# Performance work log

Measured on AMD Instinct MI355X. Metric: run time of the kernel, lower is better.

The kernel has to match this reference:

```python
import jax, jax.numpy as jnp
import numpy as np

V, D, S, L, H, R, W = 32000, 512, 1536, 4, 4, 32, 128
HFF = int(2.0 * D)
N = S + 1          # anchor node at index 0 + S tokens
K = W + 2          # anchor edge + (W+1) causal window edges
LN_EPS = 1e-5


def _layer_norm(x, g, b):
    m = jnp.mean(x, axis=-1, keepdims=True)
    v = jnp.mean((x - m) ** 2, axis=-1, keepdims=True)
    return (x - m) * jax.lax.rsqrt(v + LN_EPS) * g + b


def _neighbors():
    # windowed causal neighborhood: node i sees nodes i-W..i, plus anchor (node 0)
    pos = jnp.arange(N)
    offs = jnp.arange(-W, 1)                     # W+1 offsets
    idx_w = pos[:, None] + offs[None, :]         # [N, W+1]
    valid_w = idx_w >= 0
    idx_w = jnp.maximum(idx_w, 0)
    anchor_valid = (pos > W)[:, None]            # avoid double-counting anchor when already in window
    idx = jnp.concatenate([jnp.zeros((N, 1), idx_w.dtype), idx_w], axis=1)   # [N, K]
    mask = jnp.concatenate([anchor_valid, valid_w], axis=1)                  # [N, K]
    return idx, mask


def setup_inputs() -> dict:
    key = jax.random.key(0)
    ks = jax.random.split(key, 10)
    std = 0.02
    return {
        'input_ids': jax.random.randint(ks[0], (1, S), 0, V),
        'embed': jax.random.normal(ks[1], (V, D), jnp.float32) * std,
        'pos_emb': jax.random.normal(ks[2], (S, D), jnp.float32) * std,
        'ln_in_g': jnp.ones((D,), jnp.float32),
        'ln_in_b': jnp.zeros((D,), jnp.float32),
        'anchor_state': jnp.zeros((), jnp.float32),
        'anchor_val': jax.random.normal(ks[3], (D,), jnp.float32) * std,
        'state_w': jax.random.normal(ks[4], (D,), jnp.float32) * std,
        'state_b': jnp.zeros((), jnp.float32),
        'wq': jax.random.normal(ks[5], (L, H, D, R), jnp.float32) * std,
        'wk': jax.random.normal(ks[6], (L, H, D, R), jnp.float32) * std,
        'gate': jnp.full((L,), 0.1, jnp.float32),
        'ln_g': jnp.ones((L, D), jnp.float32),
        'ln_b': jnp.zeros((L, D), jnp.float32),
        'ffn_w1': jax.random.normal(ks[7], (L, D, HFF), jnp.float32) * std,
        'ffn_b1': jnp.zeros((L, HFF), jnp.float32),
        'ffn_w2': jax.random.normal(ks[8], (L, HFF, D), jnp.float32) * std,
        'ffn_b2': jnp.zeros((L, D), jnp.float32),
        'ln2_g': jnp.ones((L, D), jnp.float32),
        'ln2_b': jnp.zeros((L, D), jnp.float32),
    }


def reference(input_ids, embed, pos_emb, ln_in_g, ln_in_b, anchor_state, anchor_val,
              state_w, state_b, wq, wk, gate, ln_g, ln_b,
              ffn_w1, ffn_b1, ffn_w2, ffn_b2, ln2_g, ln2_b):
    B = input_ids.shape[0]
    # token embedding + learned position encoding + input norm
    tok = embed[input_ids] + pos_emb[None]                 # [B,S,D]
    tok = _layer_norm(tok, ln_in_g, ln_in_b)
    tok_state = tok @ state_w + state_b                    # [B,S] scalar state per node
    # prepend anchor node
    val = jnp.concatenate([jnp.broadcast_to(anchor_val, (B, 1, D)), tok], axis=1)       # [B,N,D]
    state = jnp.concatenate([jnp.broadcast_to(anchor_state, (B, 1)), tok_state], axis=1)  # [B,N]
    idx, mask = _neighbors()
    scale = 1.0 / np.sqrt(R)
    for l in range(L):
        # low-rank multi-head pairwise scores on windowed neighborhood
        q = jnp.einsum('bnd,hdr->bnhr', val, wq[l])
        k = jnp.einsum('bnd,hdr->bnhr', val, wk[l])
        kg = k[:, idx]                                     # [B,N,K,H,R] gather
        s = jnp.einsum('bnhr,bnkhr->bnkh', q, kg) * scale  # [B,N,K,H]
        # signed_smoothmax head aggregation
        hw = jax.nn.softmax(jnp.abs(s), axis=-1)
        a = jnp.sum(s * hw, axis=-1)                       # [B,N,K]
        # signed_abs_softmax edge compression over neighborhood
        absa = jnp.where(mask[None], jnp.abs(a), -jnp.inf)
        e = jnp.sign(a) * jax.nn.softmax(absa, axis=-1)    # masked entries -> 0 weight
        # state-weighted edges
        sg = state[:, idx]                                 # [B,N,K]
        e = e * sg
        val_g = val[:, idx]                                # [B,N,K,D]
        d_val = jnp.einsum('bnk,bnkd->bnd', e, val_g)
        d_state = jnp.sum(e, axis=-1)
        # gated residual + post-norm
        state = state + gate[l] * d_state
        val = val + gate[l] * d_val
        val = _layer_norm(val, ln_g[l], ln_b[l])
        # value feed-forward (pre-norm, residual scale 1.0)
        h = jax.nn.gelu(_layer_norm(val, ln2_g[l], ln2_b[l]) @ ffn_w1[l] + ffn_b1[l], approximate=False)
        val = val + h @ ffn_w2[l] + ffn_b2[l]
    return val
```

## Files before the change

kernel.cpp:

```cpp
#include <hip/hip_runtime.h>
#include <hip/hip_bf16.h>

namespace {

constexpr int D    = 512;
constexpr int S    = 1536;
constexpr int N    = S + 1;
constexpr int L    = 4;
constexpr int H    = 4;
constexpr int R    = 32;
constexpr int W    = 128;
constexpr int HFF  = 1024;
constexpr float EPS = 1e-5f;

constexpr int TB   = 4;
constexpr int NB4  = (N + TB - 1) / TB;
constexpr int SP   = 133;
constexpr int SPAD = 136;

typedef __attribute__((ext_vector_type(8))) short short8;
typedef __attribute__((ext_vector_type(4))) float floatx4;

__device__ inline ushort f2bf(float x){
  __hip_bfloat16 h = __float2bfloat16(x);
  return *reinterpret_cast<ushort*>(&h);
}
__device__ inline float bf2f(uint u){
  union { uint u; float f; } c; c.u = u << 16; return c.f;
}

__device__ inline float wave_sum(float v){
#pragma unroll
  for (int o = 32; o; o >>= 1) v += __shfl_xor(v, o, 64);
  return v;
}
__device__ inline float wave_max(float v){
#pragma unroll
  for (int o = 32; o; o >>= 1) v = fmaxf(v, __shfl_xor(v, o, 64));
  return v;
}
__device__ inline float block_sum(float v, float* scr){
  v = wave_sum(v);
  __syncthreads();
  if ((threadIdx.x & 63) == 0) scr[threadIdx.x >> 6] = v;
  __syncthreads();
  return scr[0] + scr[1] + scr[2] + scr[3];
}

__global__ __launch_bounds__(256) void pack_wqk_bf(const float* __restrict__ wq,
                                                   const float* __restrict__ wk,
                                                   ushort* __restrict__ out){
  int i = blockIdx.x * 256 + threadIdx.x;
  int d = i & 511;
  int c = (i >> 9) & 255;
  int l = i >> 17;
  int cc = c & 127;
  int h = cc >> 5, r = cc & 31;
  const float* src = (c < 128) ? wq : wk;
  out[i] = f2bf(src[((l * H + h) * D + d) * R + r]);
}

__global__ __launch_bounds__(256) void transpose_bf(const float* __restrict__ src,
                                                    ushort* __restrict__ dst,
                                                    int rows, int cols){
  __shared__ float tile[32][33];
  const float* s = src + (size_t)blockIdx.z * rows * cols;
  ushort* d = dst + (size_t)blockIdx.z * rows * cols;
  int c0 = blockIdx.x * 32, r0 = blockIdx.y * 32;
  int tx = threadIdx.x & 31, ty = threadIdx.x >> 5;
  for (int rr = ty; rr < 32; rr += 8)
    tile[rr][tx] = s[(size_t)(r0 + rr) * cols + c0 + tx];
  __syncthreads();
  for (int rr = ty; rr < 32; rr += 8)
    d[(size_t)(c0 + rr) * rows + r0 + tx] = f2bf(tile[tx][rr]);
}

__global__ __launch_bounds__(256) void embed_ln_kernel(
    const int* __restrict__ ids, const float* __restrict__ embed,
    const float* __restrict__ pos, const float* __restrict__ g,
    const float* __restrict__ b, const float* __restrict__ anchor_val,
    const float* __restrict__ anchor_state, const float* __restrict__ state_w,
    const float* __restrict__ state_b, float* __restrict__ val,
    ushort* __restrict__ valbf, float* __restrict__ state)
{
  __shared__ float scr[4];
  int n = blockIdx.x, t = threadIdx.x;
  if (n == 0){
    float a0 = anchor_val[t], a1 = anchor_val[t + 256];
    val[t] = a0; val[t + 256] = a1;
    valbf[t] = f2bf(a0); valbf[t + 256] = f2bf(a1);
    if (t == 0) state[0] = anchor_state[0];
    return;
  }
  int tp = n - 1;
  int id = ids[tp];
  float x0 = embed[(size_t)id * D + t]       + pos[tp * D + t];
  float x1 = embed[(size_t)id * D + t + 256] + pos[tp * D + t + 256];
  float mean = block_sum(x0 + x1, scr) * (1.f / D);
  float var  = block_sum(x0 * x0 + x1 * x1, scr) * (1.f / D) - mean * mean;
  float rs   = rsqrtf(var + EPS);
  float y0 = (x0 - mean) * rs * g[t]       + b[t];
  float y1 = (x1 - mean) * rs * g[t + 256] + b[t + 256];
  val[n * D + t]       = y0;
  val[n * D + t + 256] = y1;
  valbf[n * D + t]       = f2bf(y0);
  valbf[n * D + t + 256] = f2bf(y1);
  float ts = block_sum(y0 * state_w[t] + y1 * state_w[t + 256], scr);
  if (t == 0) state[n] = ts + state_b[0];
}

template<int ACT>
__global__ __launch_bounds__(256) void gemm_bf16(
    const ushort* __restrict__ A, const ushort* __restrict__ Bt,
    const float* __restrict__ bias, const float* __restrict__ resid,
    float* __restrict__ C, ushort* __restrict__ Cbf,
    int M, int Kd, int Nc)
{
  constexpr int SLAB = 272;
  __shared__ ushort As[8 * SLAB];
  __shared__ ushort Bs[8 * SLAB];
  int row0 = blockIdx.y * 32;
  int col0 = blockIdx.x * 32;
  int t = threadIdx.x;
  int lane = t & 63, w = t >> 6;
  int wr = w & 1, wc = w >> 1;
  int q = lane >> 4, lm = lane & 15;

  int srow = t >> 3, skb = t & 7;
  int arow = min(row0 + srow, M - 1);
  const ushort* ag = A  + (size_t)arow * Kd + skb * 8;
  const ushort* bg = Bt + (size_t)(col0 + srow) * Kd + skb * 8;
  ushort* as = &As[skb * SLAB + srow * 8];
  ushort* bs = &Bs[skb * SLAB + srow * 8];

  const ushort* ar = &As[(wr * 16 + lm) * 8];
  const ushort* br = &Bs[(wc * 16 + lm) * 8];

  floatx4 acc = {0.f, 0.f, 0.f, 0.f};

  for (int k0 = 0; k0 < Kd; k0 += 64){
    uint4 av = *(const uint4*)(ag + k0);
    uint4 bv = *(const uint4*)(bg + k0);
    *(uint4*)as = av;
    *(uint4*)bs = bv;
    __syncthreads();
#pragma unroll
    for (int kk = 0; kk < 2; ++kk){
      short8 a = *(const short8*)(ar + (kk * 4 + q) * SLAB);
      short8 b = *(const short8*)(br + (kk * 4 + q) * SLAB);
      acc = __builtin_amdgcn_mfma_f32_16x16x32_bf16(a, b, acc, 0, 0, 0);
    }
    __syncthreads();
  }

  int col = col0 + wc * 16 + lm;
#pragma unroll
  for (int r = 0; r < 4; ++r){
    int row = row0 + wr * 16 + q * 4 + r;
    if (row >= M) continue;
    float v = acc[r] + (bias ? bias[col] : 0.f);
    if (ACT == 1) v = 0.5f * v * (1.f + erff(v * 0.70710678118654752f));
    if (resid) v += resid[(size_t)row * Nc + col];
    size_t o = (size_t)row * Nc + col;
    if (C)   C[o] = v;
    if (Cbf) Cbf[o] = f2bf(v);
  }
}

__global__ __launch_bounds__(256) void attn4_kernel(
    const ushort* __restrict__ qkbf, const float* __restrict__ val0,
    const ushort* __restrict__ val0bf, const float* __restrict__ state_in,
    float* __restrict__ val1, ushort* __restrict__ x2bf,
    float* __restrict__ state_out,
    const float* __restrict__ gate_p, const float* __restrict__ lng,
    const float* __restrict__ lnb, const float* __restrict__ ln2g,
    const float* __restrict__ ln2b)
{
  __shared__ float kg[64 * SPAD];
  __shared__ float qsh[TB * 128];
  __shared__ float ssh[16 * SPAD];
  __shared__ float ash[TB * SPAD];
  const int n0 = blockIdx.x * TB;
  const int t = threadIdx.x;
  const int w = t >> 6, l = t & 63;
  const float gate = gate_p[0];
  const float scale = 0.17677669529663687f;

#pragma unroll
  for (int i = t; i < TB * 128; i += 256){
    int it = i >> 7, ch = i & 127;
    int gr = min(n0 + it, N - 1);
    qsh[i] = bf2f((uint)qkbf[(size_t)gr * 256 + ch]);
  }

  for (int half = 0; half < 2; ++half){
    for (int i = t; i < SP * 16; i += 256){
      int c = i >> 4, c4 = i & 15;
      int g = (c == 132) ? 0 : min(max(n0 - W + c, 0), N - 1);
      uint2 v = *(const uint2*)&qkbf[(size_t)g * 256 + 128 + half * 64 + c4 * 4];
      int ch = c4 * 4;
      kg[(ch + 0) * SPAD + c] = bf2f(v.x & 0xffffu);
      kg[(ch + 1) * SPAD + c] = bf2f(v.x >> 16);
      kg[(ch + 2) * SPAD + c] = bf2f(v.y & 0xffffu);
      kg[(ch + 3) * SPAD + c] = bf2f(v.y >> 16);
    }
    __syncthreads();
    for (int tk = t; tk < TB * 2 * SP; tk += 256){
      int c = tk % SP;
      int th = tk / SP;
      int tok = th & 3, hh = th >> 2;
      int h = half * 2 + hh;
      const float* qs = &qsh[tok * 128 + h * 32];
      const float* ks = &kg[hh * 32 * SPAD + c];
      float acc = 0.f;
#pragma unroll
      for (int r = 0; r < 32; ++r) acc += qs[r] * ks[r * SPAD];
      ssh[(tok * 4 + h) * SPAD + c] = acc * scale;
    }
    __syncthreads();
  }

  for (int i = t; i < TB * SP; i += 256){
    int tok = i / SP, c = i - tok * SP;
    const float* sr = &ssh[tok * 4 * SPAD + c];
    float s0 = sr[0], s1 = sr[SPAD], s2 = sr[2 * SPAD], s3 = sr[3 * SPAD];
    float a0 = fabsf(s0), a1 = fabsf(s1), a2 = fabsf(s2), a3 = fabsf(s3);
    float m = fmaxf(fmaxf(a0, a1), fmaxf(a2, a3));
    float w0 = expf(a0 - m), w1 = expf(a1 - m), w2 = expf(a2 - m), w3 = expf(a3 - m);
    ash[tok * SPAD + c] = (s0 * w0 + s1 * w1 + s2 * w2 + s3 * w3) / (w0 + w1 + w2 + w3);
  }
  __syncthreads();

  {
    const int n = n0 + w;
    float* arow = &ash[w * SPAD];
    float a0 = arow[l];
    float a1 = arow[64 + l];
    float a2 = (l < 5) ? arow[128 + l] : 0.f;
    bool ok0 = (l >= w) && (n0 - W + l >= 0);
    bool ok1 = (n0 - W + 64 + l >= 0);
    bool ok2;
    if (l < 4)       ok2 = (l <= w);
    else if (l == 4) ok2 = (n > W);
    else             ok2 = false;
    float cand = -3.4e38f;
    if (ok0) cand = fabsf(a0);
    if (ok1) cand = fmaxf(cand, fabsf(a1));
    if (ok2) cand = fmaxf(cand, fabsf(a2));
    float m = wave_max(cand);
    float e0 = ok0 ? expf(fabsf(a0) - m) : 0.f;
    float e1 = ok1 ? expf(fabsf(a1) - m) : 0.f;
    float e2 = ok2 ? expf(fabsf(a2) - m) : 0.f;
    float inv = 1.f / wave_sum(e0 + e1 + e2);
    int g0 = min(max(n0 - W + l, 0), N - 1);
    int g1 = min(max(n0 - W + 64 + l, 0), N - 1);
    int g2 = (l < 4) ? min(n0 + l, N - 1) : 0;
    float sg0 = (a0 > 0.f) ? 1.f : ((a0 < 0.f) ? -1.f : 0.f);
    float sg1 = (a1 > 0.f) ? 1.f : ((a1 < 0.f) ? -1.f : 0.f);
    float sg2 = (a2 > 0.f) ? 1.f : ((a2 < 0.f) ? -1.f : 0.f);
    float t0 = sg0 * e0 * inv * state_in[g0];
    float t1 = sg1 * e1 * inv * state_in[g1];
    float t2 = (l < 5) ? sg2 * e2 * inv * state_in[g2] : 0.f;
    arow[l] = t0;
    arow[64 + l] = t1;
    if (l < 5) arow[128 + l] = t2;
    float ds = wave_sum(t0 + t1 + t2);
    if (l == 0 && n < N) state_out[n] = state_in[n] + gate * ds;
  }
  __syncthreads();

  float acc[TB][2];
#pragma unroll
  for (int k = 0; k < TB; ++k){ acc[k][0] = 0.f; acc[k][1] = 0.f; }
  {
    const int d0 = 2 * t;
    for (int c = 0; c < SP; ++c){
      int g = (c == 132) ? 0 : min(max(n0 - W + c, 0), N - 1);
      uint v = *(const uint*)&val0bf[(size_t)g * D + d0];
      float vx = bf2f(v & 0xffffu), vy = bf2f(v >> 16);
#pragma unroll
      for (int k = 0; k < TB; ++k){
        float e = ash[k * SPAD + c];
        acc[k][0] += e * vx;
        acc[k][1] += e * vy;
      }
    }
  }
  float* xbuf = kg;
  {
    const int d0 = 2 * t;
#pragma unroll
    for (int k = 0; k < TB; ++k){
      int nc = min(n0 + k, N - 1);
      float2 vv = *(const float2*)&val0[(size_t)nc * D + d0];
      xbuf[k * 520 + d0]     = vv.x + gate * acc[k][0];
      xbuf[k * 520 + d0 + 1] = vv.y + gate * acc[k][1];
    }
  }
  __syncthreads();

  {
    const int n = n0 + w;
    const int d = l * 8;
    const float* xr = &xbuf[w * 520 + d];
    float x[8];
#pragma unroll
    for (int j = 0; j < 8; ++j) x[j] = xr[j];
    float s1 = 0.f, s2 = 0.f;
#pragma unroll
    for (int j = 0; j < 8; ++j){ s1 += x[j]; s2 += x[j] * x[j]; }
    s1 = wave_sum(s1); s2 = wave_sum(s2);
    float mean = s1 * (1.f / D);
    float var  = s2 * (1.f / D) - mean * mean;
    float rs   = rsqrtf(var + EPS);
    float y[8];
    float u1 = 0.f, u2 = 0.f;
#pragma unroll
    for (int j = 0; j < 8; ++j){
      float yv = (x[j] - mean) * rs * lng[d + j] + lnb[d + j];
      y[j] = yv; u1 += yv; u2 += yv * yv;
    }
    u1 = wave_sum(u1); u2 = wave_sum(u2);
    float mean2 = u1 * (1.f / D);
    float var2  = u2 * (1.f / D) - mean2 * mean2;
    float rs2   = rsqrtf(var2 + EPS);
    if (n < N){
      *(float4*)&val1[(size_t)n * D + d]     = make_float4(y[0], y[1], y[2], y[3]);
      *(float4*)&val1[(size_t)n * D + d + 4] = make_float4(y[4], y[5], y[6], y[7]);
      uint4 pk;
      uint z0 = f2bf((y[0] - mean2) * rs2 * ln2g[d + 0] + ln2b[d + 0]);
      uint z1 = f2bf((y[1] - mean2) * rs2 * ln2g[d + 1] + ln2b[d + 1]);
      uint z2 = f2bf((y[2] - mean2) * rs2 * ln2g[d + 2] + ln2b[d + 2]);
      uint z3 = f2bf((y[3] - mean2) * rs2 * ln2g[d + 3] + ln2b[d + 3]);
      uint z4 = f2bf((y[4] - mean2) * rs2 * ln2g[d + 4] + ln2b[d + 4]);
      uint z5 = f2bf((y[5] - mean2) * rs2 * ln2g[d + 5] + ln2b[d + 5]);
      uint z6 = f2bf((y[6] - mean2) * rs2 * ln2g[d + 6] + ln2b[d + 6]);
      uint z7 = f2bf((y[7] - mean2) * rs2 * ln2g[d + 7] + ln2b[d + 7]);
      pk.x = z0 | (z1 << 16); pk.y = z2 | (z3 << 16);
      pk.z = z4 | (z5 << 16); pk.w = z6 | (z7 << 16);
      *(uint4*)&x2bf[(size_t)n * D + d] = pk;
    }
  }
}

}

extern "C" void kernel_launch(void* const* d_in, const int* in_sizes, int n_in,
                              void* d_out, int out_size, void* d_ws, size_t ws_size,
                              hipStream_t stream)
{
  (void)in_sizes; (void)n_in; (void)out_size; (void)ws_size;
  const int*   ids          = (const int*)d_in[0];
  const float* embed        = (const float*)d_in[1];
  const float* pos_emb      = (const float*)d_in[2];
  const float* ln_in_g      = (const float*)d_in[3];
  const float* ln_in_b      = (const float*)d_in[4];
  const float* anchor_state = (const float*)d_in[5];
  const float* anchor_val   = (const float*)d_in[6];
  const float* state_w      = (const float*)d_in[7];
  const float* state_b      = (const float*)d_in[8];
  const float* wq           = (const float*)d_in[9];
  const float* wk           = (const float*)d_in[10];
  const float* gate         = (const float*)d_in[11];
  const float* ln_g         = (const float*)d_in[12];
  const float* ln_b         = (const float*)d_in[13];
  const float* ffn_w1       = (const float*)d_in[14];
  const float* ffn_b1       = (const float*)d_in[15];
  const float* ffn_w2       = (const float*)d_in[16];
  const float* ffn_b2       = (const float*)d_in[17];
  const float* ln2_g        = (const float*)d_in[18];
  const float* ln2_b        = (const float*)d_in[19];
  float* out = (float*)d_out;

  float* wsf  = (float*)d_ws;
  float* val0 = wsf;  wsf += (size_t)N * D;
  float* val1 = wsf;  wsf += (size_t)N * D;
  ushort* wsu   = (ushort*)wsf;
  ushort* val0bf = wsu;  wsu += (size_t)N * D;
  ushort* x2bf   = wsu;  wsu += (size_t)N * D;
  ushort* hbf    = wsu;  wsu += (size_t)N * HFF;
  ushort* qkbf   = wsu;  wsu += (size_t)N * 256;
  ushort* wqkbf  = wsu;  wsu += (size_t)L * 256 * D;
  ushort* w1t    = wsu;  wsu += (size_t)L * HFF * D;
  ushort* w2t    = wsu;  wsu += (size_t)L * HFF * D;
  float* st0 = (float*)wsu;
  float* st1 = st0 + N;

  pack_wqk_bf<<<L * 512, 256, 0, stream>>>(wq, wk, wqkbf);
  transpose_bf<<<dim3(HFF / 32, D / 32, L), 256, 0, stream>>>(ffn_w1, w1t, D, HFF);
  transpose_bf<<<dim3(D / 32, HFF / 32, L), 256, 0, stream>>>(ffn_w2, w2t, HFF, D);
  embed_ln_kernel<<<N, 256, 0, stream>>>(ids, embed, pos_emb, ln_in_g, ln_in_b,
                                         anchor_val, anchor_state, state_w,
                                         state_b, val0, val0bf, st0);

  float* sin_  = st0;
  float* sout_ = st1;
  const int MT32 = (N + 31) / 32;
  for (int l = 0; l < L; ++l){
    gemm_bf16<0><<<dim3(256 / 32, MT32), 256, 0, stream>>>(
        val0bf, wqkbf + (size_t)l * 256 * D, nullptr, nullptr,
        nullptr, qkbf, N, D, 256);
    attn4_kernel<<<NB4, 256, 0, stream>>>(qkbf, val0, val0bf, sin_, val1, x2bf,
                                          sout_, gate + l, ln_g + l * D,
                                          ln_b + l * D, ln2_g + l * D,
                                          ln2_b + l * D);
    gemm_bf16<1><<<dim3(HFF / 32, MT32), 256, 0, stream>>>(
        x2bf, w1t + (size_t)l * HFF * D, ffn_b1 + l * HFF, nullptr,
        nullptr, hbf, N, D, HFF);
    float* dst = (l == L - 1) ? out : val0;
    gemm_bf16<0><<<dim3(D / 32, MT32), 256, 0, stream>>>(
        hbf, w2t + (size_t)l * HFF * D, ffn_b2 + l * D, val1,
        dst, val0bf, N, HFF, D);
    float* tmp = sin_; sin_ = sout_; sout_ = tmp;
  }
}
```

Before: 370.7 us.

## Enlarge GEMM tiles to 64x64, merge setup kernels, repad attention smem

The bf16 MFMA GEMM moves from 32x32 to 64x64 output tiles, with each wave computing a 2x2 grid of 16x16 MFMA blocks. This is meant to raise operand reuse per LDS load and cut redundant global traffic. The four setup launches (weight pack, two transposes, embed+LN) become one grid-stride kernel, removing launch overhead. The attention smem padding also changes from 136 to 137 to avoid bank conflicts. Larger tiles shrink the grid (for example 4x25 blocks for the QK projection), which may leave many CUs idle on a 256-CU part.

```diff
diff --git a/kernel.cpp b/kernel.cpp
--- a/kernel.cpp
+++ b/kernel.cpp
@@ -1,5 +1,6 @@
 #include <hip/hip_runtime.h>
 #include <hip/hip_bf16.h>
+#include <stdint.h>
 
 namespace {
 
@@ -16,7 +17,10 @@
 constexpr int TB   = 4;
 constexpr int NB4  = (N + TB - 1) / TB;
 constexpr int SP   = 133;
-constexpr int SPAD = 136;
+constexpr int SPAD = 137;
+
+constexpr int GS2  = 1024;
+constexpr int SLAB2 = 528;
 
 typedef __attribute__((ext_vector_type(8))) short short8;
 typedef __attribute__((ext_vector_type(4))) float floatx4;
@@ -47,123 +51,161 @@
   return scr[0] + scr[1] + scr[2] + scr[3];
 }
 
-__global__ __launch_bounds__(256) void pack_wqk_bf(const float* __restrict__ wq,
-                                                   const float* __restrict__ wk,
-                                                   ushort* __restrict__ out){
-  int i = blockIdx.x * 256 + threadIdx.x;
-  int d = i & 511;
-  int c = (i >> 9) & 255;
-  int l = i >> 17;
-  int cc = c & 127;
-  int h = cc >> 5, r = cc & 31;
-  const float* src = (c < 128) ? wq : wk;
-  out[i] = f2bf(src[((l * H + h) * D + d) * R + r]);
-}
-
-__global__ __launch_bounds__(256) void transpose_bf(const float* __restrict__ src,
-                                                    ushort* __restrict__ dst,
-                                                    int rows, int cols){
-  __shared__ float tile[32][33];
-  const float* s = src + (size_t)blockIdx.z * rows * cols;
-  ushort* d = dst + (size_t)blockIdx.z * rows * cols;
-  int c0 = blockIdx.x * 32, r0 = blockIdx.y * 32;
-  int tx = threadIdx.x & 31, ty = threadIdx.x >> 5;
-  for (int rr = ty; rr < 32; rr += 8)
-    tile[rr][tx] = s[(size_t)(r0 + rr) * cols + c0 + tx];
-  __syncthreads();
-  for (int rr = ty; rr < 32; rr += 8)
-    d[(size_t)(c0 + rr) * rows + r0 + tx] = f2bf(tile[tx][rr]);
-}
-
-__global__ __launch_bounds__(256) void embed_ln_kernel(
+__global__ __launch_bounds__(256) void setup_kernel(
     const int* __restrict__ ids, const float* __restrict__ embed,
     const float* __restrict__ pos, const float* __restrict__ g,
     const float* __restrict__ b, const float* __restrict__ anchor_val,
     const float* __restrict__ anchor_state, const float* __restrict__ state_w,
     const float* __restrict__ state_b, float* __restrict__ val,
-    ushort* __restrict__ valbf, float* __restrict__ state)
+    ushort* __restrict__ valbf, float* __restrict__ state,
+    const float* __restrict__ wq, const float* __restrict__ wk,
+    ushort* __restrict__ wqkbf,
+    const float* __restrict__ ffn_w1, const float* __restrict__ ffn_w2,
+    ushort* __restrict__ w1t, ushort* __restrict__ w2t)
 {
   __shared__ float scr[4];
-  int n = blockIdx.x, t = threadIdx.x;
-  if (n == 0){
-    float a0 = anchor_val[t], a1 = anchor_val[t + 256];
-    val[t] = a0; val[t + 256] = a1;
-    valbf[t] = f2bf(a0); valbf[t + 256] = f2bf(a1);
-    if (t == 0) state[0] = anchor_state[0];
-    return;
-  }
-  int tp = n - 1;
-  int id = ids[tp];
-  float x0 = embed[(size_t)id * D + t]       + pos[tp * D + t];
-  float x1 = embed[(size_t)id * D + t + 256] + pos[tp * D + t + 256];
-  float mean = block_sum(x0 + x1, scr) * (1.f / D);
-  float var  = block_sum(x0 * x0 + x1 * x1, scr) * (1.f / D) - mean * mean;
-  float rs   = rsqrtf(var + EPS);
-  float y0 = (x0 - mean) * rs * g[t]       + b[t];
-  float y1 = (x1 - mean) * rs * g[t + 256] + b[t + 256];
-  val[n * D + t]       = y0;
-  val[n * D + t + 256] = y1;
-  valbf[n * D + t]       = f2bf(y0);
-  valbf[n * D + t + 256] = f2bf(y1);
-  float ts = block_sum(y0 * state_w[t] + y1 * state_w[t + 256], scr);
-  if (t == 0) state[n] = ts + state_b[0];
+  __shared__ float tile[32 * 33];
+  const int t = threadIdx.x;
+
+  for (int n = blockIdx.x; n < N; n += GS2){
+    if (n == 0){
+      float a0 = anchor_val[t], a1 = anchor_val[t + 256];
+      val[t] = a0; val[t + 256] = a1;
+      valbf[t] = f2bf(a0); valbf[t + 256] = f2bf(a1);
+      if (t == 0) state[0] = anchor_state[0];
+      continue;
+    }
+    int tp = n - 1;
+    int id = ids[tp];
+    float x0 = embed[(size_t)id * D + t]       + pos[tp * D + t];
+    float x1 = embed[(size_t)id * D + t + 256] + pos[tp * D + t + 256];
+    float mean = block_sum(x0 + x1, scr) * (1.f / D);
+    float var  = block_sum(x0 * x0 + x1 * x1, scr) * (1.f / D) - mean * mean;
+    float rs   = rsqrtf(var + EPS);
+    float y0 = (x0 - mean) * rs * g[t]       + b[t];
+    float y1 = (x1 - mean) * rs * g[t + 256] + b[t + 256];
+    val[n * D + t]       = y0;
+    val[n * D + t + 256] = y1;
+    valbf[n * D + t]       = f2bf(y0);
+    valbf[n * D + t + 256] = f2bf(y1);
+    float ts = block_sum(y0 * state_w[t] + y1 * state_w[t + 256], scr);
+    if (t == 0) state[n] = ts + state_b[0];
+  }
+
+  for (int i = blockIdx.x * 256 + t; i < L * 256 * D; i += GS2 * 256){
+    int d = i & 511;
+    int c = (i >> 9) & 255;
+    int l = i >> 17;
+    int cc = c & 127;
+    int h = cc >> 5, r = cc & 31;
+    const float* src = (c < 128) ? wq : wk;
+    wqkbf[i] = f2bf(src[((l * H + h) * D + d) * R + r]);
+  }
+  __syncthreads();
+
+  const int tx = t & 31, ty = t >> 5;
+  for (int tl = blockIdx.x; tl < 2 * L * 512; tl += GS2){
+    const float* s; ushort* dd; int rows, cols, c0, r0;
+    if (tl < 2048){
+      int ll = tl >> 9, i = tl & 511;
+      rows = D; cols = HFF;
+      s  = ffn_w1 + (size_t)ll * D * HFF;
+      dd = w1t   + (size_t)ll * D * HFF;
+      c0 = (i & 31) << 5; r0 = (i >> 5) << 5;
+    } else {
+      int tl2 = tl - 2048;
+      int ll = tl2 >> 9, i = tl2 & 511;
+      rows = HFF; cols = D;
+      s  = ffn_w2 + (size_t)ll * D * HFF;
+      dd = w2t   + (size_t)ll * D * HFF;
+      c0 = (i & 15) << 5; r0 = (i >> 4) << 5;
+    }
+    __syncthreads();
+    for (int rr = ty; rr < 32; rr += 8)
+      tile[rr * 33 + tx] = s[(size_t)(r0 + rr) * cols + c0 + tx];
+    __syncthreads();
+    for (int rr = ty; rr < 32; rr += 8)
+      dd[(size_t)(c0 + rr) * rows + r0 + tx] = f2bf(tile[tx * 33 + rr]);
+  }
 }
 
 template<int ACT>
-__global__ __launch_bounds__(256) void gemm_bf16(
+__global__ __launch_bounds__(256) void gemm64(
     const ushort* __restrict__ A, const ushort* __restrict__ Bt,
     const float* __restrict__ bias, const float* __restrict__ resid,
     float* __restrict__ C, ushort* __restrict__ Cbf,
     int M, int Kd, int Nc)
 {
-  constexpr int SLAB = 272;
-  __shared__ ushort As[8 * SLAB];
-  __shared__ ushort Bs[8 * SLAB];
-  int row0 = blockIdx.y * 32;
-  int col0 = blockIdx.x * 32;
-  int t = threadIdx.x;
-  int lane = t & 63, w = t >> 6;
-  int wr = w & 1, wc = w >> 1;
-  int q = lane >> 4, lm = lane & 15;
-
-  int srow = t >> 3, skb = t & 7;
-  int arow = min(row0 + srow, M - 1);
-  const ushort* ag = A  + (size_t)arow * Kd + skb * 8;
-  const ushort* bg = Bt + (size_t)(col0 + srow) * Kd + skb * 8;
-  ushort* as = &As[skb * SLAB + srow * 8];
-  ushort* bs = &Bs[skb * SLAB + srow * 8];
-
-  const ushort* ar = &As[(wr * 16 + lm) * 8];
-  const ushort* br = &Bs[(wc * 16 + lm) * 8];
-
-  floatx4 acc = {0.f, 0.f, 0.f, 0.f};
+  __shared__ ushort As[8 * SLAB2];
+  __shared__ ushort Bs[8 * SLAB2];
+  const int row0 = blockIdx.y * 64;
+  const int col0 = blockIdx.x * 64;
+  const int t = threadIdx.x;
+  const int lane = t & 63, w = t >> 6;
+  const int wr = w & 1, wc = w >> 1;
+  const int q = lane >> 4, lm = lane & 15;
+
+  const int srow = t >> 3, skb = t & 7;
+  int ar0 = min(row0 + srow,      M - 1);
+  int ar1 = min(row0 + srow + 32, M - 1);
+  const ushort* ag0 = A  + (size_t)ar0 * Kd + skb * 8;
+  const ushort* ag1 = A  + (size_t)ar1 * Kd + skb * 8;
+  const ushort* bg0 = Bt + (size_t)(col0 + srow) * Kd + skb * 8;
+  const ushort* bg1 = Bt + (size_t)(col0 + srow + 32) * Kd + skb * 8;
+  ushort* as0 = &As[skb * SLAB2 + srow * 8];
+  ushort* as1 = &As[skb * SLAB2 + (srow + 32) * 8];
+  ushort* bs0 = &Bs[skb * SLAB2 + srow * 8];
+  ushort* bs1 = &Bs[skb * SLAB2 + (srow + 32) * 8];
+
+  const ushort* arp = &As[(wr * 32 + lm) * 8];
+  const ushort* brp = &Bs[(wc * 32 + lm) * 8];
+
+  floatx4 acc[2][2];
+#pragma unroll
+  for (int m = 0; m < 2; ++m)
+#pragma unroll
+    for (int n = 0; n < 2; ++n) acc[m][n] = {0.f, 0.f, 0.f, 0.f};
 
   for (int k0 = 0; k0 < Kd; k0 += 64){
-    uint4 av = *(const uint4*)(ag + k0);
-    uint4 bv = *(const uint4*)(bg + k0);
-    *(uint4*)as = av;
-    *(uint4*)bs = bv;
+    uint4 a0 = *(const uint4*)(ag0 + k0);
+    uint4 a1 = *(const uint4*)(ag1 + k0);
+    uint4 b0 = *(const uint4*)(bg0 + k0);
+    uint4 b1 = *(const uint4*)(bg1 + k0);
+    *(uint4*)as0 = a0; *(uint4*)as1 = a1;
+    *(uint4*)bs0 = b0; *(uint4*)bs1 = b1;
     __syncthreads();
 #pragma unroll
     for (int kk = 0; kk < 2; ++kk){
-      short8 a = *(const short8*)(ar + (kk * 4 + q) * SLAB);
-      short8 b = *(const short8*)(br + (kk * 4 + q) * SLAB);
-      acc = __builtin_amdgcn_mfma_f32_16x16x32_bf16(a, b, acc, 0, 0, 0);
-    }
-    __syncthreads();
-  }
-
-  int col = col0 + wc * 16 + lm;
-#pragma unroll
-  for (int r = 0; r < 4; ++r){
-    int row = row0 + wr * 16 + q * 4 + r;
-    if (row >= M) continue;
-    float v = acc[r] + (bias ? bias[col] : 0.f);
-    if (ACT == 1) v = 0.5f * v * (1.f + erff(v * 0.70710678118654752f));
-    if (resid) v += resid[(size_t)row * Nc + col];
-    size_t o = (size_t)row * Nc + col;
-    if (C)   C[o] = v;
-    if (Cbf) Cbf[o] = f2bf(v);
+      const int kb = (kk * 4 + q) * SLAB2;
+      short8 am0 = *(const short8*)(arp + kb);
+      short8 am1 = *(const short8*)(arp + kb + 16 * 8);
+      short8 bn0 = *(const short8*)(brp + kb);
+      short8 bn1 = *(const short8*)(brp + kb + 16 * 8);
+      acc[0][0] = __builtin_amdgcn_mfma_f32_16x16x32_bf16(am0, bn0, acc[0][0], 0, 0, 0);
+      acc[0][1] = __builtin_amdgcn_mfma_f32_16x16x32_bf16(am0, bn1, acc[0][1], 0, 0, 0);
+      acc[1][0] = __builtin_amdgcn_mfma_f32_16x16x32_bf16(am1, bn0, acc[1][0], 0, 0, 0);
+      acc[1][1] = __builtin_amdgcn_mfma_f32_16x16x32_bf16(am1, bn1, acc[1][1], 0, 0, 0);
+    }
+    __syncthreads();
+  }
+
+#pragma unroll
+  for (int m = 0; m < 2; ++m){
+#pragma unroll
+    for (int n = 0; n < 2; ++n){
+      int col = col0 + wc * 32 + n * 16 + lm;
+#pragma unroll
+      for (int r = 0; r < 4; ++r){
+        int row = row0 + wr * 32 + m * 16 + q * 4 + r;
+        if (row >= M) continue;
+        float v = acc[m][n][r] + (bias ? bias[col] : 0.f);
+        if (ACT == 1) v = 0.5f * v * (1.f + erff(v * 0.70710678118654752f));
+        if (resid) v += resid[(size_t)row * Nc + col];
+        size_t o = (size_t)row * Nc + col;
+        if (C)   C[o] = v;
+        if (Cbf) Cbf[o] = f2bf(v);
+      }
+    }
   }
 }
 
@@ -386,29 +428,27 @@
   float* st0 = (float*)wsu;
   float* st1 = st0 + N;
 
-  pack_wqk_bf<<<L * 512, 256, 0, stream>>>(wq, wk, wqkbf);
-  transpose_bf<<<dim3(HFF / 32, D / 32, L), 256, 0, stream>>>(ffn_w1, w1t, D, HFF);
-  transpose_bf<<<dim3(D / 32, HFF / 32, L), 256, 0, stream>>>(ffn_w2, w2t, HFF, D);
-  embed_ln_kernel<<<N, 256, 0, stream>>>(ids, embed, pos_emb, ln_in_g, ln_in_b,
-                                         anchor_val, anchor_state, state_w,
-                                         state_b, val0, val0bf, st0);
+  setup_kernel<<<GS2, 256, 0, stream>>>(
+      ids, embed, pos_emb, ln_in_g, ln_in_b, anchor_val, anchor_state,
+      state_w, state_b, val0, val0bf, st0,
+      wq, wk, wqkbf, ffn_w1, ffn_w2, w1t, w2t);
 
   float* sin_  = st0;
   float* sout_ = st1;
-  const int MT32 = (N + 31) / 32;
+  const int MT64 = (N + 63) / 64;
   for (int l = 0; l < L; ++l){
-    gemm_bf16<0><<<dim3(256 / 32, MT32), 256, 0, stream>>>(
+    gemm64<0><<<dim3(256 / 64, MT64), 256, 0, stream>>>(
         val0bf, wqkbf + (size_t)l * 256 * D, nullptr, nullptr,
         nullptr, qkbf, N, D, 256);
     attn4_kernel<<<NB4, 256, 0, stream>>>(qkbf, val0, val0bf, sin_, val1, x2bf,
                                           sout_, gate + l, ln_g + l * D,
                                           ln_b + l * D, ln2_g + l * D,
                                           ln2_b + l * D);
-    gemm_bf16<1><<<dim3(HFF / 32, MT32), 256, 0, stream>>>(
+    gemm64<1><<<dim3(HFF / 64, MT64), 256, 0, stream>>>(
         x2bf, w1t + (size_t)l * HFF * D, ffn_b1 + l * HFF, nullptr,
         nullptr, hbf, N, D, HFF);
     float* dst = (l == L - 1) ? out : val0;
-    gemm_bf16<0><<<dim3(D / 32, MT32), 256, 0, stream>>>(
+    gemm64<0><<<dim3(D / 64, MT64), 256, 0, stream>>>(
         hbf, w2t + (size_t)l * HFF * D, ffn_b2 + l * D, val1,
         dst, val0bf, N, HFF, D);
     float* tmp = sin_; sin_ = sout_; sout_ = tmp;
```

New measurement: 400.0 us. 7.9% more time.
